# Optimization experiments

Measured on AMD Instinct MI355X. Metric: run time of the kernel, lower is better.

## Reference

```python
import jax, jax.numpy as jnp
import numpy as np

N = 100000      # nodes
E = 800000      # directed edges per branch
HID = 128
FOUT = 128
HEADS = 2
LAYERS = 3      # convlayer
JK_LAYERS = 3
H2 = (JK_LAYERS * HID) // 2   # PyG JK-LSTM hidden size = 192
N_AA = 26
N_SS = 3


def setup_inputs() -> dict:
    key = jax.random.key(0)
    ks = iter(jax.random.split(key, 32))
    def nrm(shape, scale=0.05):
        return jax.random.normal(next(ks), shape, dtype=jnp.float32) * scale
    return {
        "x_idx": jax.random.randint(next(ks), (N, 2), 0, N_SS),
        "x_flt": jax.random.normal(next(ks), (N, 5), dtype=jnp.float32),
        "edge_index_l": jax.random.randint(next(ks), (2, E), 0, N),
        "edge_index_r": jax.random.randint(next(ks), (2, E), 0, N),
        "emb_aa": nrm((2, N_AA, HID - 5)),          # [branch, vocab, hid-5]
        "emb_ss": nrm((2, N_SS, HID - 5)),
        "conv_W": nrm((2, LAYERS, HID, HEADS * HID)),
        "conv_att_src": nrm((2, LAYERS, HEADS, HID)),
        "conv_att_dst": nrm((2, LAYERS, HEADS, HID)),
        "conv_bias": nrm((2, LAYERS, HID)),
        "lstm_Wih": nrm((2, 2, 4 * H2, HID)),        # [branch, direction, 4H2, hid]
        "lstm_Whh": nrm((2, 2, 4 * H2, H2)),
        "lstm_bih": nrm((2, 2, 4 * H2)),
        "lstm_bhh": nrm((2, 2, 4 * H2)),
        "jk_att_W": nrm((2, 2 * H2)),
        "jk_att_b": nrm((2,)),
        "dummy_W": nrm((2, HID, HID)),
        "dummy_b": nrm((2, HID)),
        "fin_W": nrm((4, HID, FOUT)),
        "fin_b": nrm((4, FOUT)),
        "last_W": nrm((FOUT,)),                      # Linear(fout,1,bias=False)
    }


def _gat_conv(x, src, dst, W, att_src, att_dst, bias):
    # PyG GATConv, concat=False (mean over heads), leaky_relu slope 0.2
    n = x.shape[0]
    h, c = att_src.shape
    xh = (x @ W).reshape(n, h, c)                         # [N,H,C]
    a_src = jnp.einsum('nhc,hc->nh', xh, att_src)
    a_dst = jnp.einsum('nhc,hc->nh', xh, att_dst)
    e = jax.nn.leaky_relu(a_src[src] + a_dst[dst], 0.2)   # [E,H]
    m = jax.ops.segment_max(e, dst, num_segments=n)
    ex = jnp.exp(e - m[dst])
    denom = jax.ops.segment_sum(ex, dst, num_segments=n)
    alpha = ex / (denom[dst] + 1e-16)                     # segment softmax over dst
    out = jax.ops.segment_sum(xh[src] * alpha[:, :, None], dst, num_segments=n)
    return out.mean(axis=1) + bias                        # [N,C]


def _lstm_dir(xs, Wih, Whh, bih, bhh, reverse):
    # xs: [L,N,C]; single-layer LSTM, torch gate order i,f,g,o
    n = xs.shape[1]
    h2 = Whh.shape[1]
    b = bih + bhh
    def cell(carry, xt):
        h, c = carry
        g = xt @ Wih.T + h @ Whh.T + b
        i, f, gg, o = jnp.split(g, 4, axis=-1)
        c = jax.nn.sigmoid(f) * c + jax.nn.sigmoid(i) * jnp.tanh(gg)
        h = jax.nn.sigmoid(o) * jnp.tanh(c)
        return (h, c), h
    init = (jnp.zeros((n, h2), xs.dtype), jnp.zeros((n, h2), xs.dtype))
    _, hs = jax.lax.scan(cell, init, xs, reverse=reverse)
    return hs  # [L,N,H2]


def _jk(xs, Wih, Whh, bih, bhh, att_w, att_b):
    # PyG JumpingKnowledge('lstm'): bi-LSTM over layer axis + scalar attention
    hf = _lstm_dir(xs, Wih[0], Whh[0], bih[0], bhh[0], False)
    hb = _lstm_dir(xs, Wih[1], Whh[1], bih[1], bhh[1], True)
    h = jnp.concatenate([hf, hb], axis=-1)                # [L,N,2H2]
    a = jax.nn.softmax(jnp.einsum('lnh,h->ln', h, att_w) + att_b, axis=0)
    return (xs * a[..., None]).sum(axis=0)                # [N,C]


def _forward(x_idx, x_flt, edge_index_l, edge_index_r, emb_aa, emb_ss,
             conv_W, conv_att_src, conv_att_dst, conv_bias,
             lstm_Wih, lstm_Whh, lstm_bih, lstm_bhh, jk_att_W, jk_att_b,
             dummy_W, dummy_b, fin_W, fin_b, last_W):
    n = x_idx.shape[0]
    loops = jnp.arange(n)  # GATConv add_self_loops=True
    src_l = jnp.concatenate([edge_index_l[0], loops]); dst_l = jnp.concatenate([edge_index_l[1], loops])
    src_r = jnp.concatenate([edge_index_r[0], loops]); dst_r = jnp.concatenate([edge_index_r[1], loops])
    x_l = jnp.concatenate([emb_aa[0][x_idx[:, 0]] + emb_ss[0][x_idx[:, 1]], x_flt], axis=1)
    x_r = jnp.concatenate([emb_aa[1][x_idx[:, 0]] + emb_ss[1][x_idx[:, 1]], x_flt], axis=1)
    xs_l, xs_r = [], []
    for i in range(LAYERS):
        mean = (x_l + x_r) * 0.5
        o_l = mean + jax.nn.relu(_gat_conv(x_l, src_l, dst_l, conv_W[0, i], conv_att_src[0, i], conv_att_dst[0, i], conv_bias[0, i]))
        o_r = mean + jax.nn.relu(_gat_conv(x_r, src_r, dst_r, conv_W[1, i], conv_att_src[1, i], conv_att_dst[1, i], conv_bias[1, i]))
        x_l, x_r = o_l, o_r
        xs_l.append(x_l); xs_r.append(x_r)
    jk_l = _jk(jnp.stack(xs_l), lstm_Wih[0], lstm_Whh[0], lstm_bih[0], lstm_bhh[0], jk_att_W[0], jk_att_b[0])
    jk_r = _jk(jnp.stack(xs_r), lstm_Wih[1], lstm_Whh[1], lstm_bih[1], lstm_bhh[1], jk_att_W[1], jk_att_b[1])
    sq_l = jk_l @ dummy_W[0] + dummy_b[0]
    sq_r = jk_r @ dummy_W[1] + dummy_b[1]
    feats = [jk_l, sq_l, jk_r, sq_r]
    outs = [feats[i] @ fin_W[i] + fin_b[i] for i in range(4)]
    alpha = jax.nn.softmax(jnp.stack([o @ last_W for o in outs], axis=1), axis=1)  # [N,4]
    nodeemb = sum(outs[i] * alpha[:, i:i + 1] for i in range(4))
    return nodeemb


def reference(x_idx, x_flt, edge_index_l, edge_index_r, emb_aa, emb_ss,
              conv_W, conv_att_src, conv_att_dst, conv_bias,
              lstm_Wih, lstm_Whh, lstm_bih, lstm_bhh, jk_att_W, jk_att_b,
              dummy_W, dummy_b, fin_W, fin_b, last_W):
    return _forward(x_idx, x_flt, edge_index_l, edge_index_r, emb_aa, emb_ss,
                    conv_W, conv_att_src, conv_att_dst, conv_bias,
                    lstm_Wih, lstm_Whh, lstm_bih, lstm_bhh, jk_att_W, jk_att_b,
                    dummy_W, dummy_b, fin_W, fin_b, last_W)
```

## Files before the change

### kernel.cpp

```cpp
#include <hip/hip_runtime.h>
#include <cstddef>
#include <cstdint>

#define N_NODES 100000
#define N_EDGES 800000
#define EL_TOT  900000
#define HID 128
#define H2  192
#define G4  768
#define CH3 50000
#define BK  32
#define LDST 32
#define SCANB 98

typedef unsigned short bf16;
typedef __attribute__((ext_vector_type(8))) short bf16x8v;
typedef __attribute__((ext_vector_type(4))) float f32x4v;

#define AS1 __attribute__((address_space(1)))
#define AS3 __attribute__((address_space(3)))

__device__ __forceinline__ void async16(const bf16* g, bf16* l) {
    __builtin_amdgcn_global_load_lds((AS1 void*)g, (AS3 void*)l, 16, 0, 0);
}


__device__ __forceinline__ float b2f(bf16 u) {
    return __uint_as_float(((unsigned)u) << 16);
}
__device__ __forceinline__ bf16 f2b(float f) {
    unsigned u = __float_as_uint(f);
    u += 0x7FFFu + ((u >> 16) & 1u);
    return (bf16)(u >> 16);
}
__device__ __forceinline__ void stE(float* p, size_t i, float v) { p[i] = v; }
__device__ __forceinline__ void stE(bf16* p, size_t i, float v) { p[i] = f2b(v); }
__device__ __forceinline__ float ftanh(float x) {
    float cx = fminf(fmaxf(x, -15.f), 15.f);
    float e = __expf(2.f * cx);
    return (e - 1.f) / (e + 1.f);
}

__device__ __forceinline__ float x0_val(int c, int ia, int is_, int n,
                                        const float* __restrict__ embA,
                                        const float* __restrict__ embS,
                                        const float* __restrict__ xflt) {
    return (c < 123) ? (embA[ia * 123 + c] + embS[is_ * 123 + c])
                     : xflt[n * 5 + (c - 123)];
}

__device__ __forceinline__ int lstm_perm(int j) {
    int w = j & 63, tt = j >> 6;
    return (w >> 4) * 192 + tt * 16 + (w & 15);
}

__device__ __forceinline__ bool swz_tile(int R, int ntile, int& bm0, int& nt) {
    const int id = blockIdx.x;
    const int xcd = id & 7;
    const int s = id >> 3;
    nt = s % ntile;
    const int yp = (s / ntile) * 8 + xcd;
    if (yp * 128 >= R) return false;
    bm0 = yp * 128;
    return true;
}
static inline int swz_grid(int R, int ntile) {
    int panels = (R + 127) / 128;
    return 8 * ntile * ((panels + 7) / 8);
}


__global__ void sentinel_kernel(float* out, int n, float val) {
    int t = blockIdx.x * blockDim.x + threadIdx.x;
    if (t < n) out[t] = val;
}

__global__ void bsum_perm_kernel(const float* __restrict__ bih,
                                 const float* __restrict__ bhh,
                                 float* __restrict__ bsum) {
    int t = blockIdx.x * blockDim.x + threadIdx.x;
    if (t >= 4 * G4) return;
    int d = t / G4, j = t % G4;
    int orig = lstm_perm(j);
    bsum[t] = bih[d * G4 + orig] + bhh[d * G4 + orig];
}

__global__ void lstm_w_perm_kernel(const float* __restrict__ in,
                                   bf16* __restrict__ out, int K) {
    long long t = (long long)blockIdx.x * blockDim.x + threadIdx.x;
    long long tot = 4LL * G4 * K;
    if (t >= tot) return;
    int k = (int)(t % K);
    int j = (int)((t / K) % G4);
    int d = (int)(t / ((long long)G4 * K));
    int orig = lstm_perm(j);
    out[t] = f2b(in[((size_t)d * G4 + orig) * K + k]);
}

__global__ void trans_kernel(const float* __restrict__ in, bf16* __restrict__ out,
                             int batch, int K, int M) {
    long long t = (long long)blockIdx.x * blockDim.x + threadIdx.x;
    long long tot = (long long)batch * K * M;
    if (t >= tot) return;
    int per = K * M;
    int bt = (int)(t / per);
    int rem = (int)(t % per);
    int m = rem / K, k = rem % K;
    out[t] = f2b(in[(size_t)bt * per + (size_t)k * M + m]);
}


__global__ void deg_kernel(const int* __restrict__ dst, int* __restrict__ deg) {
    int t = blockIdx.x * blockDim.x + threadIdx.x;
    if (t >= EL_TOT) return;
    int d = (t < N_EDGES) ? dst[t] : (t - N_EDGES);
    atomicAdd(&deg[d], 1);
}

__global__ void scan1_kernel(const int* __restrict__ deg0, const int* __restrict__ deg1,
                             int* __restrict__ tmp0, int* __restrict__ tmp1,
                             int* __restrict__ bsums) {
    __shared__ int sdata[1024];
    const int b = blockIdx.y;
    const int* deg = b ? deg1 : deg0;
    int* tmp = b ? tmp1 : tmp0;
    int i = blockIdx.x * 1024 + threadIdx.x;
    int v = (i < N_NODES) ? deg[i] : 0;
    sdata[threadIdx.x] = v;
    __syncthreads();
    for (int off = 1; off < 1024; off <<= 1) {
        int t = (threadIdx.x >= (unsigned)off) ? sdata[threadIdx.x - off] : 0;
        __syncthreads();
        sdata[threadIdx.x] += t;
        __syncthreads();
    }
    if (i < N_NODES) tmp[i] = sdata[threadIdx.x];
    if (threadIdx.x == 1023) bsums[b * SCANB + blockIdx.x] = sdata[1023];
}

__global__ void scan2_kernel(int* __restrict__ bsums) {
    int b = threadIdx.x;
    if (b < 2) {
        int c = 0;
        for (int k = 0; k < SCANB; ++k) {
            int t = bsums[b * SCANB + k];
            bsums[b * SCANB + k] = c;
            c += t;
        }
    }
}

__global__ void scan3_kernel(const int* __restrict__ bsums,
                             const int* __restrict__ deg0, const int* __restrict__ deg1,
                             const int* __restrict__ tmp0, const int* __restrict__ tmp1,
                             int* __restrict__ offs0, int* __restrict__ offs1,
                             int* __restrict__ pos0, int* __restrict__ pos1) {
    const int b = blockIdx.y;
    const int* deg = b ? deg1 : deg0;
    const int* tmp = b ? tmp1 : tmp0;
    int* offs = b ? offs1 : offs0;
    int* pos = b ? pos1 : pos0;
    int carry = bsums[b * SCANB + blockIdx.x];
    int i = blockIdx.x * 1024 + threadIdx.x;
    if (i < N_NODES) {
        int inc = tmp[i] + carry;
        offs[i + 1] = inc;
        pos[i] = inc - deg[i];
    }
    if (i == 0) offs[0] = 0;
}

__global__ void fill_kernel(const int* __restrict__ srcrow,
                            const int* __restrict__ dstrow,
                            int* __restrict__ pos, int* __restrict__ srcs) {
    int t = blockIdx.x * blockDim.x + threadIdx.x;
    if (t >= EL_TOT) return;
    int s, d;
    if (t < N_EDGES) { s = srcrow[t]; d = dstrow[t]; }
    else             { s = d = t - N_EDGES; }
    int p = atomicAdd(&pos[d], 1);
    srcs[p] = s;
}

template<typename TC>
__device__ __forceinline__ void gemm128_body(
    const bf16* __restrict__ A1, const bf16* __restrict__ B1, int K1,
    TC* __restrict__ C, const float* __restrict__ bias, int R, int M,
    int bm0, int bn0, const float* __restrict__ as_, float* __restrict__ asrc) {
    __shared__ bf16 As[2][128 * LDST];
    __shared__ bf16 Bs[2][128 * LDST];
    const int tid = threadIdx.x;
    const int lane = tid & 63;
    const int wave = tid >> 6;
    const int wm = (wave & 1) * 64, wn = (wave >> 1) * 64;
    const int l15 = lane & 15;
    const int q8 = (lane >> 4) * 8;
    const int lr = lane >> 2;
    const int lc = (lane & 3) * 8;

    f32x4v acc[4][4];
#pragma unroll
    for (int i = 0; i < 4; ++i)
#pragma unroll
        for (int j = 0; j < 4; ++j) acc[i][j] = (f32x4v)(0.0f);

    const int ns = K1 / BK;
    auto stage = [&](int buf, int s) {
        const int k0 = s * BK;
#pragma unroll
        for (int rnd = 0; rnd < 2; ++rnd) {
            const int rbase = wave * 16 + rnd * 64;
            const int row = rbase + lr;
            int ga = bm0 + row; ga = (ga < R) ? ga : (R - 1);
            async16(A1 + (size_t)ga * K1 + k0 + lc, &As[buf][rbase * LDST]);
            async16(B1 + (size_t)(bn0 + row) * K1 + k0 + lc, &Bs[buf][rbase * LDST]);
        }
    };

    stage(0, 0);
    __syncthreads();
    for (int s = 0; s < ns; ++s) {
        const int cur = s & 1;
        if (s + 1 < ns) stage(cur ^ 1, s + 1);
        bf16x8v af[4], bfv[4];
#pragma unroll
        for (int i = 0; i < 4; ++i) {
            af[i]  = *(const bf16x8v*)&As[cur][(wm + i * 16 + l15) * LDST + q8];
            bfv[i] = *(const bf16x8v*)&Bs[cur][(wn + i * 16 + l15) * LDST + q8];
        }
#pragma unroll
        for (int i = 0; i < 4; ++i)
#pragma unroll
            for (int j = 0; j < 4; ++j)
                acc[i][j] = __builtin_amdgcn_mfma_f32_16x16x32_bf16(
                    af[i], bfv[j], acc[i][j], 0, 0, 0);
        __syncthreads();
    }

    const int head = bn0 >> 7;
#pragma unroll
    for (int i = 0; i < 4; ++i) {
        const int row0 = bm0 + wm + i * 16 + (lane >> 4) * 4;
        if (as_) {
            float rs[4] = {0.f, 0.f, 0.f, 0.f};
#pragma unroll
            for (int j = 0; j < 4; ++j) {
                const float w = as_[bn0 + wn + j * 16 + l15];
#pragma unroll
                for (int r = 0; r < 4; ++r) rs[r] += w * acc[i][j][r];
            }
#pragma unroll
            for (int m = 1; m < 16; m <<= 1)
#pragma unroll
                for (int r = 0; r < 4; ++r) rs[r] += __shfl_xor(rs[r], m);
            if (l15 == 0) {
#pragma unroll
                for (int r = 0; r < 4; ++r) {
                    const int gr = row0 + r;
                    if (gr < R) asrc[2 * gr + head] = rs[r];
                }
            }
        }
#pragma unroll
        for (int j = 0; j < 4; ++j) {
            const int col = bn0 + wn + j * 16 + l15;
            const float bv = bias ? bias[col] : 0.f;
#pragma unroll
            for (int r = 0; r < 4; ++r) {
                const int gr = row0 + r;
                if (gr < R) stE(C, (size_t)gr * M + col, acc[i][j][r] + bv);
            }
        }
    }
}

template<typename TC>
__global__ __launch_bounds__(256) void mfma_gemm_kernel(
    const bf16* __restrict__ A1, const bf16* __restrict__ B1, int K1,
    TC* __restrict__ C, const float* __restrict__ bias, int R, int M,
    const float* __restrict__ as_, float* __restrict__ asrc) {
    int bm0, nt;
    if (!swz_tile(R, M >> 7, bm0, nt)) return;
    gemm128_body<TC>(A1, B1, K1, C, bias, R, M, bm0, nt * 128, as_, asrc);
}

template<typename TC>
__global__ __launch_bounds__(256) void mfma_gemm_b_kernel(
    const bf16* a0, const bf16* a1, const bf16* a2, const bf16* a3,
    const bf16* __restrict__ Bbase,
    TC* c0, TC* c1, TC* c2, TC* c3,
    const float* __restrict__ bias, int R) {
    int bm0, nt;
    if (!swz_tile(R, 1, bm0, nt)) return;
    const int y = blockIdx.y;
    const bf16* A1 = (y == 0) ? a0 : (y == 1) ? a1 : (y == 2) ? a2 : a3;
    TC* C = (y == 0) ? c0 : (y == 1) ? c1 : (y == 2) ? c2 : c3;
    gemm128_body<TC>(A1, Bbase + (size_t)y * 128 * 128, 128, C,
                     bias + (size_t)y * 128, R, 128, bm0, 0, nullptr, nullptr);
}

__global__ __launch_bounds__(256) void lstm_gemm_kernel(
    const bf16* __restrict__ A1, const bf16* __restrict__ B1,
    const bf16* __restrict__ A2, const bf16* __restrict__ B2,
    const float* __restrict__ bias, bf16* __restrict__ c_state,
    bf16* __restrict__ h_out, const float* __restrict__ aw,
    float* __restrict__ score, int first, int last, int R) {
    __shared__ bf16 As[2][128 * LDST];
    __shared__ bf16 Bs[2][128 * LDST];
    int bm0, nt;
    if (!swz_tile(R, G4 >> 7, bm0, nt)) return;
    const int bn0 = nt * 128;
    const int tid = threadIdx.x;
    const int lane = tid & 63;
    const int wave = tid >> 6;
    const int wm = (wave & 1) * 64, wn = (wave >> 1) * 64;
    const int l15 = lane & 15;
    const int q = lane >> 4;
    const int q8 = q * 8;
    const int lr = lane >> 2;
    const int lc = (lane & 3) * 8;

    f32x4v acc[4][4];
#pragma unroll
    for (int i = 0; i < 4; ++i)
#pragma unroll
        for (int j = 0; j < 4; ++j) acc[i][j] = (f32x4v)(0.0f);

    const int n1 = HID / BK;
    const int ns = n1 + (first ? 0 : (H2 / BK));

    auto stage = [&](int buf, int s) {
        const bf16* Ap; const bf16* Bp; int K, k0;
        if (s < n1) { Ap = A1; Bp = B1; K = HID; k0 = s * BK; }
        else        { Ap = A2; Bp = B2; K = H2;  k0 = (s - n1) * BK; }
#pragma unroll
        for (int rnd = 0; rnd < 2; ++rnd) {
            const int rbase = wave * 16 + rnd * 64;
            const int row = rbase + lr;
            int ga = bm0 + row; ga = (ga < R) ? ga : (R - 1);
            async16(Ap + (size_t)ga * K + k0 + lc, &As[buf][rbase * LDST]);
            async16(Bp + (size_t)(bn0 + row) * K + k0 + lc, &Bs[buf][rbase * LDST]);
        }
    };

    stage(0, 0);
    __syncthreads();
    for (int s = 0; s < ns; ++s) {
        const int cur = s & 1;
        if (s + 1 < ns) stage(cur ^ 1, s + 1);
        bf16x8v af[4], bfv[4];
#pragma unroll
        for (int i = 0; i < 4; ++i) {
            af[i]  = *(const bf16x8v*)&As[cur][(wm + i * 16 + l15) * LDST + q8];
            bfv[i] = *(const bf16x8v*)&Bs[cur][(wn + i * 16 + l15) * LDST + q8];
        }
#pragma unroll
        for (int i = 0; i < 4; ++i)
#pragma unroll
            for (int j = 0; j < 4; ++j)
                acc[i][j] = __builtin_amdgcn_mfma_f32_16x16x32_bf16(
                    af[i], bfv[j], acc[i][j], 0, 0, 0);
        __syncthreads();
    }

    const int u = ((bn0 + wn) >> 6) * 16 + l15;
    const float awu = aw[u];
    float bv[4];
#pragma unroll
    for (int j = 0; j < 4; ++j) bv[j] = bias[bn0 + wn + j * 16 + l15];
    float psum[4][4];
#pragma unroll
    for (int i = 0; i < 4; ++i) {
        const int row0 = bm0 + wm + i * 16 + q * 4;
#pragma unroll
        for (int r = 0; r < 4; ++r) {
            const int gr = row0 + r;
            const bool ok = gr < R;
            float ig = acc[i][0][r] + bv[0];
            float fg = acc[i][1][r] + bv[1];
            float gg = acc[i][2][r] + bv[2];
            float og = acc[i][3][r] + bv[3];
            float si = 1.f / (1.f + __expf(-ig));
            float sf = 1.f / (1.f + __expf(-fg));
            float so = 1.f / (1.f + __expf(-og));
            float co = (ok && !first) ? b2f(c_state[(size_t)gr * H2 + u]) : 0.f;
            float cn = sf * co + si * ftanh(gg);
            float hn = so * ftanh(cn);
            if (ok && !last) {
                c_state[(size_t)gr * H2 + u] = f2b(cn);
                h_out[(size_t)gr * H2 + u] = f2b(hn);
            }
            psum[i][r] = hn * awu;
        }
    }
#pragma unroll
    for (int m = 1; m < 16; m <<= 1)
#pragma unroll
        for (int i = 0; i < 4; ++i)
#pragma unroll
            for (int r = 0; r < 4; ++r)
                psum[i][r] += __shfl_xor(psum[i][r], m);
    if (l15 == 0) {
#pragma unroll
        for (int i = 0; i < 4; ++i)
#pragma unroll
            for (int r = 0; r < 4; ++r) {
                const int gr = bm0 + wm + i * 16 + q * 4 + r;
                if (gr < R) atomicAdd(&score[gr], psum[i][r]);
            }
    }
}

__global__ __launch_bounds__(256) void mfma_gemm_x0_kernel(
    const int* __restrict__ xidx, const float* __restrict__ xflt,
    const float* __restrict__ embA, const float* __restrict__ embS,
    const bf16* __restrict__ B1, bf16* __restrict__ C, int R, int M,
    const float* __restrict__ as_, float* __restrict__ asrc) {
    __shared__ bf16 As[128 * LDST];
    __shared__ bf16 Bs[128 * LDST];
    int bm0, nt;
    if (!swz_tile(R, M >> 7, bm0, nt)) return;
    const int bn0 = nt * 128;
    const int tid = threadIdx.x;
    const int lane = tid & 63;
    const int wave = tid >> 6;
    const int wm = (wave & 1) * 64, wn = (wave >> 1) * 64;
    const int l15 = lane & 15;
    const int q8 = (lane >> 4) * 8;
    const int srow = tid >> 2;
    const int scol = (tid & 3) * 8;
    const int lr = lane >> 2;
    const int lc = (lane & 3) * 8;

    f32x4v acc[4][4];
#pragma unroll
    for (int i = 0; i < 4; ++i)
#pragma unroll
        for (int j = 0; j < 4; ++j) acc[i][j] = (f32x4v)(0.0f);

    for (int k0 = 0; k0 < 128; k0 += BK) {
#pragma unroll
        for (int rnd = 0; rnd < 2; ++rnd) {
            {
                int row = srow + rnd * 64;
                int ga = bm0 + row; ga = (ga < R) ? ga : (R - 1);
                int ia = xidx[2 * ga], is_ = xidx[2 * ga + 1];
                bf16 tmp[8];
#pragma unroll
                for (int t = 0; t < 8; ++t)
                    tmp[t] = f2b(x0_val(k0 + scol + t, ia, is_, ga, embA, embS, xflt));
                *(int4*)&As[row * LDST + scol] = *(const int4*)tmp;
            }
            {
                const int rbase = wave * 16 + rnd * 64;
                int row = rbase + lr;
                async16(B1 + (size_t)(bn0 + row) * 128 + k0 + lc, &Bs[rbase * LDST]);
            }
        }
        __syncthreads();
        bf16x8v af[4], bfv[4];
#pragma unroll
        for (int i = 0; i < 4; ++i) {
            af[i]  = *(const bf16x8v*)&As[(wm + i * 16 + l15) * LDST + q8];
            bfv[i] = *(const bf16x8v*)&Bs[(wn + i * 16 + l15) * LDST + q8];
        }
#pragma unroll
        for (int i = 0; i < 4; ++i)
#pragma unroll
            for (int j = 0; j < 4; ++j)
                acc[i][j] = __builtin_amdgcn_mfma_f32_16x16x32_bf16(
                    af[i], bfv[j], acc[i][j], 0, 0, 0);
        __syncthreads();
    }
    const int head = bn0 >> 7;
#pragma unroll
    for (int i = 0; i < 4; ++i) {
        const int row0 = bm0 + wm + i * 16 + (lane >> 4) * 4;
        {
            float rs[4] = {0.f, 0.f, 0.f, 0.f};
#pragma unroll
            for (int j = 0; j < 4; ++j) {
                const float w = as_[bn0 + wn + j * 16 + l15];
#pragma unroll
                for (int r = 0; r < 4; ++r) rs[r] += w * acc[i][j][r];
            }
#pragma unroll
            for (int m = 1; m < 16; m <<= 1)
#pragma unroll
                for (int r = 0; r < 4; ++r) rs[r] += __shfl_xor(rs[r], m);
            if (l15 == 0) {
#pragma unroll
                for (int r = 0; r < 4; ++r) {
                    const int gr = row0 + r;
                    if (gr < R) asrc[2 * gr + head] = rs[r];
                }
            }
        }
#pragma unroll
        for (int j = 0; j < 4; ++j) {
            const int col = bn0 + wn + j * 16 + l15;
#pragma unroll
            for (int r = 0; r < 4; ++r) {
                const int gr = row0 + r;
                if (gr < R) C[(size_t)gr * M + col] = f2b(acc[i][j][r]);
            }
        }
    }
}


__device__ __forceinline__ float lrelu02(float x) { return x > 0.f ? x : 0.2f * x; }

__global__ __launch_bounds__(256) void agg_kernel(
    const bf16* __restrict__ xh, const float* __restrict__ asrc,
    const float* __restrict__ ad_, const int* __restrict__ offs,
    const int* __restrict__ srcs,
    const bf16* __restrict__ xprev_l, const bf16* __restrict__ xprev_r,
    const int* __restrict__ xidx, const float* __restrict__ xflt,
    const float* __restrict__ embAl, const float* __restrict__ embSl,
    const float* __restrict__ embAr, const float* __restrict__ embSr,
    const float* __restrict__ bias, bf16* __restrict__ outx) {
    int n = (blockIdx.x * blockDim.x + threadIdx.x) >> 6;
    int lane = threadIdx.x & 63;
    if (n >= N_NODES) return;
    const int start = offs[n], end = offs[n + 1];
    const int l15 = lane & 15;
    const int g = lane >> 4;

    float d0, d1;
    {
        uint2 v = *(const uint2*)(xh + (size_t)n * 256 + lane * 4);
        float p = ad_[lane * 4 + 0] * b2f((bf16)(v.x & 0xffffu))
                + ad_[lane * 4 + 1] * b2f((bf16)(v.x >> 16))
                + ad_[lane * 4 + 2] * b2f((bf16)(v.y & 0xffffu))
                + ad_[lane * 4 + 3] * b2f((bf16)(v.y >> 16));
        for (int o = 1; o < 32; o <<= 1) p += __shfl_xor(p, o);
        d0 = __shfl(p, 0);
        d1 = __shfl(p, 32);
    }

    float acc0[8] = {0, 0, 0, 0, 0, 0, 0, 0};
    float acc1[8] = {0, 0, 0, 0, 0, 0, 0, 0};
    float ds0 = 0.f, ds1 = 0.f;
#pragma unroll 2
    for (int j = start; j < end; j += 4) {
        int e = j + g;
        if (e < end) {
            int s = srcs[e];
            float2 a2 = *(const float2*)(asrc + 2 * s);
            float al0 = __expf(lrelu02(a2.x + d0));
            float al1 = __expf(lrelu02(a2.y + d1));
            if (l15 == 0) { ds0 += al0; ds1 += al1; }
            const bf16* row = xh + (size_t)s * 256 + l15 * 8;
            int4 v0 = *(const int4*)row;
            int4 v1 = *(const int4*)(row + 128);
            const int* w0 = (const int*)&v0;
            const int* w1 = (const int*)&v1;
#pragma unroll
            for (int t = 0; t < 4; ++t) {
                acc0[2 * t]     += __uint_as_float(((unsigned)w0[t]) << 16) * al0;
                acc0[2 * t + 1] += __uint_as_float(((unsigned)w0[t]) & 0xffff0000u) * al0;
                acc1[2 * t]     += __uint_as_float(((unsigned)w1[t]) << 16) * al1;
                acc1[2 * t + 1] += __uint_as_float(((unsigned)w1[t]) & 0xffff0000u) * al1;
            }
        }
    }
#pragma unroll
    for (int t = 0; t < 8; ++t) {
        acc0[t] += __shfl_xor(acc0[t], 16); acc0[t] += __shfl_xor(acc0[t], 32);
        acc1[t] += __shfl_xor(acc1[t], 16); acc1[t] += __shfl_xor(acc1[t], 32);
    }
    ds0 += __shfl_xor(ds0, 16); ds0 += __shfl_xor(ds0, 32);
    ds1 += __shfl_xor(ds1, 16); ds1 += __shfl_xor(ds1, 32);
    ds0 = __shfl(ds0, 0); ds1 = __shfl(ds1, 0);
    const float inv0 = 1.f / (ds0 + 1e-16f);
    const float inv1 = 1.f / (ds1 + 1e-16f);
    float accm[8];
#pragma unroll
    for (int t = 0; t < 8; ++t)
        accm[t] = 0.5f * (acc0[t] * inv0 + acc1[t] * inv1);

    if (lane < 16) {
        const int c0 = l15 * 8;
        const size_t base = (size_t)n * HID + c0;
        float xm[8];
        if (xidx) {
            int ia = xidx[2 * n], is_ = xidx[2 * n + 1];
#pragma unroll
            for (int t = 0; t < 8; ++t)
                xm[t] = 0.5f * (x0_val(c0 + t, ia, is_, n, embAl, embSl, xflt) +
                                x0_val(c0 + t, ia, is_, n, embAr, embSr, xflt));
        } else {
            int4 vl = *(const int4*)(xprev_l + base);
            int4 vr = *(const int4*)(xprev_r + base);
            const int* wl = (const int*)&vl;
            const int* wr = (const int*)&vr;
#pragma unroll
            for (int t = 0; t < 4; ++t) {
                xm[2 * t] = 0.5f * (__uint_as_float(((unsigned)wl[t]) << 16) +
                                    __uint_as_float(((unsigned)wr[t]) << 16));
                xm[2 * t + 1] = 0.5f * (__uint_as_float(((unsigned)wl[t]) & 0xffff0000u) +
                                        __uint_as_float(((unsigned)wr[t]) & 0xffff0000u));
            }
        }
        bf16 res[8];
#pragma unroll
        for (int t = 0; t < 8; ++t)
            res[t] = f2b(xm[t] + fmaxf(0.f, accm[t] + bias[c0 + t]));
        *(int4*)(outx + base) = *(const int4*)res;
    }
}


__global__ __launch_bounds__(256) void jkfin_kernel(
    const float* __restrict__ sb, const bf16* __restrict__ xs0,
    const bf16* __restrict__ xs1, const bf16* __restrict__ xs2,
    bf16* __restrict__ jk) {
    int w = (blockIdx.x * blockDim.x + threadIdx.x) >> 6;
    int lane = threadIdx.x & 63;
    if (w >= N_NODES) return;
    float s0 = sb[w], s1 = sb[N_NODES + w], s2 = sb[2 * N_NODES + w];
    float m = fmaxf(s0, fmaxf(s1, s2));
    float a0 = __expf(s0 - m), a1 = __expf(s1 - m), a2 = __expf(s2 - m);
    float inv = 1.f / (a0 + a1 + a2);
    a0 *= inv; a1 *= inv; a2 *= inv;
    size_t gn = (size_t)w * HID + lane * 2;
#pragma unroll
    for (int t = 0; t < 2; ++t) {
        float v0 = b2f(xs0[gn + t]);
        float v1 = b2f(xs1[gn + t]);
        float v2 = b2f(xs2[gn + t]);
        jk[gn + t] = f2b(v0 * a0 + v1 * a1 + v2 * a2);
    }
}

__global__ __launch_bounds__(256) void final_kernel(
    const float* __restrict__ o0, const float* __restrict__ o1,
    const float* __restrict__ o2, const float* __restrict__ o3,
    const float* __restrict__ lw, float* __restrict__ out, int nloc, long long c3off) {
    int w = (blockIdx.x * blockDim.x + threadIdx.x) >> 6;
    int lane = threadIdx.x & 63;
    if (w >= nloc) return;
    size_t base = (size_t)w * HID;
    float w0 = lw[lane], w1 = lw[64 + lane];
    const float* op[4] = {o0, o1, o2, o3};
    float v[4][2];
    float s[4];
#pragma unroll
    for (int i = 0; i < 4; ++i) {
        v[i][0] = op[i][base + lane];
        v[i][1] = op[i][base + 64 + lane];
        float t = v[i][0] * w0 + v[i][1] * w1;
        for (int o = 1; o < 64; o <<= 1) t += __shfl_xor(t, o);
        s[i] = t;
    }
    float m = fmaxf(fmaxf(s[0], s[1]), fmaxf(s[2], s[3]));
    float e0 = __expf(s[0] - m), e1 = __expf(s[1] - m);
    float e2 = __expf(s[2] - m), e3 = __expf(s[3] - m);
    float inv = 1.f / (e0 + e1 + e2 + e3);
    float r0 = (v[0][0] * e0 + v[1][0] * e1 + v[2][0] * e2 + v[3][0] * e3) * inv;
    float r1 = (v[0][1] * e0 + v[1][1] * e1 + v[2][1] * e2 + v[3][1] * e3) * inv;
    size_t obase = (size_t)(c3off + w) * HID;
    out[obase + lane] = r0;
    out[obase + 64 + lane] = r1;
}


static long long align1k(long long x) { return (x + 1023) & ~1023LL; }

extern "C" void kernel_launch(void* const* d_in, const int* in_sizes, int n_in,
                              void* d_out, int out_size, void* d_ws, size_t ws_size,
                              hipStream_t stream) {
    (void)in_sizes; (void)n_in; (void)out_size;
    const int*   x_idx   = (const int*)  d_in[0];
    const float* x_flt   = (const float*)d_in[1];
    const int*   ei_l    = (const int*)  d_in[2];
    const int*   ei_r    = (const int*)  d_in[3];
    const float* emb_aa  = (const float*)d_in[4];
    const float* emb_ss  = (const float*)d_in[5];
    const float* conv_W  = (const float*)d_in[6];
    const float* att_s   = (const float*)d_in[7];
    const float* att_d   = (const float*)d_in[8];
    const float* conv_b  = (const float*)d_in[9];
    const float* Wih     = (const float*)d_in[10];
    const float* Whh     = (const float*)d_in[11];
    const float* bih     = (const float*)d_in[12];
    const float* bhh     = (const float*)d_in[13];
    const float* jkw     = (const float*)d_in[14];
    const float* dummy_W = (const float*)d_in[16];
    const float* dummy_b = (const float*)d_in[17];
    const float* fin_W   = (const float*)d_in[18];
    const float* fin_b   = (const float*)d_in[19];
    const float* last_W  = (const float*)d_in[20];
    float* out = (float*)d_out;

    const long long S = (long long)N_NODES * HID;
    char* ws = (char*)d_ws;
    long long off = 0;

    bf16* hist = (bf16*)(ws + off);  off += align1k(6 * S * 2);
    float* scores = (float*)(ws + off); off += align1k(6LL * N_NODES * 4);
    float* bsum   = (float*)(ws + off); off += align1k(4LL * G4 * 4);
    int* bsums    = (int*)(ws + off);  off += align1k(2LL * SCANB * 4);
    bf16* Wih_b   = (bf16*)(ws + off); off += align1k(4LL * G4 * HID * 2);
    bf16* Whh_b   = (bf16*)(ws + off); off += align1k(4LL * G4 * H2 * 2);
    bf16* dummyWt = (bf16*)(ws + off); off += align1k(2LL * 128 * 128 * 2);
    bf16* finWt   = (bf16*)(ws + off); off += align1k(4LL * 128 * 128 * 2);

    char* BIG = ws + off;
    const long long slot0 = align1k(2 * S * 2);
    const long long slot1 = align1k((long long)N_NODES * H2 * 2);
    const long long need = off + slot0 + slot1;

    if ((long long)ws_size < need) {
        float val = 200000.0f + (float)(ws_size >> 20);
        sentinel_kernel<<<(N_NODES * HID + 255) / 256, 256, 0, stream>>>(
            out, N_NODES * HID, val);
        return;
    }

    bf16* xh  = (bf16*)BIG;
    bf16* jkb = (bf16*)BIG;
    int* ibase = (int*)(BIG + slot0);
    int *deg[2], *offs[2], *pos[2], *srcs[2];
    long long io = 0;
    for (int b = 0; b < 2; ++b) {
        deg[b]  = ibase + io; io += N_NODES;
        offs[b] = ibase + io; io += N_NODES + 1;
        pos[b]  = ibase + io; io += N_NODES;
        srcs[b] = ibase + io; io += EL_TOT;
    }
    long long io4a = ((io * 4 + 15) & ~15LL);
    float* asrc = (float*)(BIG + slot0 + io4a);
    bf16* convWt = (bf16*)(BIG + slot0 + io4a + 2LL * N_NODES * 4);
    bf16* hA = (bf16*)BIG;
    bf16* hB = (bf16*)d_out;
    bf16* cC = (bf16*)(BIG + slot0);

    const float* embA[2] = {emb_aa, emb_aa + 26 * 123};
    const float* embS[2] = {emb_ss, emb_ss + 3 * 123};

    bsum_perm_kernel<<<12, 256, 0, stream>>>(bih, bhh, bsum);
    trans_kernel<<<(6 * 128 * 256 + 255) / 256, 256, 0, stream>>>(
        conv_W, convWt, 6, 128, 256);
    lstm_w_perm_kernel<<<(4 * G4 * HID + 255) / 256, 256, 0, stream>>>(
        Wih, Wih_b, HID);
    lstm_w_perm_kernel<<<(4 * G4 * H2 + 255) / 256, 256, 0, stream>>>(
        Whh, Whh_b, H2);
    trans_kernel<<<(2 * 128 * 128 + 255) / 256, 256, 0, stream>>>(
        dummy_W, dummyWt, 2, 128, 128);
    trans_kernel<<<(4 * 128 * 128 + 255) / 256, 256, 0, stream>>>(
        fin_W, finWt, 4, 128, 128);
    hipMemsetAsync(deg[0], 0, N_NODES * sizeof(int), stream);
    hipMemsetAsync(deg[1], 0, N_NODES * sizeof(int), stream);
    deg_kernel<<<(EL_TOT + 255) / 256, 256, 0, stream>>>(ei_l + N_EDGES, deg[0]);
    deg_kernel<<<(EL_TOT + 255) / 256, 256, 0, stream>>>(ei_r + N_EDGES, deg[1]);
    scan1_kernel<<<dim3(SCANB, 2), 1024, 0, stream>>>(
        deg[0], deg[1], pos[0], pos[1], bsums);
    scan2_kernel<<<1, 64, 0, stream>>>(bsums);
    scan3_kernel<<<dim3(SCANB, 2), 1024, 0, stream>>>(
        bsums, deg[0], deg[1], pos[0], pos[1], offs[0], offs[1], pos[0], pos[1]);
    fill_kernel<<<(EL_TOT + 255) / 256, 256, 0, stream>>>(
        ei_l, ei_l + N_EDGES, pos[0], srcs[0]);
    fill_kernel<<<(EL_TOT + 255) / 256, 256, 0, stream>>>(
        ei_r, ei_r + N_EDGES, pos[1], srcs[1]);

    for (int i = 0; i < 3; ++i) {
        for (int b = 0; b < 2; ++b) {
            const bf16* Wc = convWt + (size_t)(b * 3 + i) * 256 * 128;
            const float* as_ = att_s + (size_t)(b * 3 + i) * 2 * HID;
            if (i == 0) {
                mfma_gemm_x0_kernel<<<swz_grid(N_NODES, 2), 256, 0, stream>>>(
                    x_idx, x_flt, embA[b], embS[b], Wc, xh, N_NODES, 256,
                    as_, asrc);
            } else {
                mfma_gemm_kernel<bf16><<<swz_grid(N_NODES, 2), 256, 0, stream>>>(
                    hist + (size_t)(b * 3 + i - 1) * S, Wc, 128,
                    xh, nullptr, N_NODES, 256, as_, asrc);
            }
            const bf16* xpl = (i == 0) ? nullptr : hist + (size_t)(i - 1) * S;
            const bf16* xpr = (i == 0) ? nullptr : hist + (size_t)(3 + i - 1) * S;
            agg_kernel<<<25000, 256, 0, stream>>>(
                xh, asrc, att_d + (size_t)(b * 3 + i) * 2 * HID,
                offs[b], srcs[b], xpl, xpr,
                (i == 0) ? x_idx : nullptr, x_flt,
                embA[0], embS[0], embA[1], embS[1],
                conv_b + (size_t)(b * 3 + i) * HID, hist + (size_t)(b * 3 + i) * S);
        }
    }

    hipMemsetAsync(scores, 0, (size_t)6 * N_NODES * 4, stream);
    const int gx = swz_grid(N_NODES, 6);
    for (int b = 0; b < 2; ++b) {
        for (int dir = 0; dir < 2; ++dir) {
            const int combo = b * 2 + dir;
            const bf16* Wi = Wih_b + (size_t)combo * G4 * HID;
            const bf16* Wh = Whh_b + (size_t)combo * G4 * H2;
            const float* bs = bsum + (size_t)combo * G4;
            const float* aw = jkw + (size_t)b * 2 * H2 + (size_t)dir * H2;
            for (int st = 0; st < 3; ++st) {
                int l = dir ? (2 - st) : st;
                const bf16* A = hist + (size_t)(b * 3 + l) * S;
                const bf16* hin = (st == 0) ? nullptr : ((st & 1) ? hA : hB);
                bf16* hout = (st & 1) ? hB : hA;
                lstm_gemm_kernel<<<gx, 256, 0, stream>>>(
                    A, Wi, hin, Wh, bs, cC, hout, aw,
                    scores + (size_t)(b * 3 + l) * N_NODES,
                    st == 0 ? 1 : 0, st == 2 ? 1 : 0, N_NODES);
            }
        }
    }
    for (int b = 0; b < 2; ++b)
        jkfin_kernel<<<25000, 256, 0, stream>>>(
            scores + (size_t)b * 3 * N_NODES,
            hist + (size_t)b * 3 * S, hist + (size_t)(b * 3 + 1) * S,
            hist + (size_t)(b * 3 + 2) * S, jkb + (size_t)b * S);

    float* f3 = (float*)hist;
    bf16* jkl = jkb; bf16* jkr = jkb + S;
    for (long long c3 = 0; c3 < N_NODES; c3 += CH3) {
        int Rr = (int)((N_NODES - c3) < CH3 ? (N_NODES - c3) : CH3);
        float* o0 = f3;
        float* o1 = f3 + 1LL * CH3 * HID;
        float* o2 = f3 + 2LL * CH3 * HID;
        float* o3 = f3 + 3LL * CH3 * HID;
        bf16* sql = (bf16*)(f3 + 4LL * CH3 * HID);
        bf16* sqr = sql + (long long)CH3 * HID;
        mfma_gemm_b_kernel<bf16><<<dim3(swz_grid(Rr, 1), 2), 256, 0, stream>>>(
            jkl + c3 * HID, jkr + c3 * HID, nullptr, nullptr,
            dummyWt, sql, sqr, nullptr, nullptr, dummy_b, Rr);
        mfma_gemm_b_kernel<float><<<dim3(swz_grid(Rr, 1), 4), 256, 0, stream>>>(
            jkl + c3 * HID, sql, jkr + c3 * HID, sqr,
            finWt, o0, o1, o2, o3, fin_b, Rr);
        final_kernel<<<(Rr + 3) / 4, 256, 0, stream>>>(
            o0, o1, o2, o3, last_W, out, Rr, c3);
    }
}
```

Baseline: 2.841 ms.

## Overlap next branch's GAT GEMM with current branch's aggregation in fused launches

```diff
diff --git a/kernel.cpp b/kernel.cpp
--- a/kernel.cpp
+++ b/kernel.cpp
@@ -12,6 +12,8 @@
 #define BK  32
 #define LDST 32
 #define SCANB 98
+#define GEMM_GRID 1568
+#define AGG_GRID 25000
 
 typedef unsigned short bf16;
 typedef __attribute__((ext_vector_type(8))) short bf16x8v;
@@ -54,8 +56,7 @@
     return (w >> 4) * 192 + tt * 16 + (w & 15);
 }
 
-__device__ __forceinline__ bool swz_tile(int R, int ntile, int& bm0, int& nt) {
-    const int id = blockIdx.x;
+__device__ __forceinline__ bool swz_tile(int id, int R, int ntile, int& bm0, int& nt) {
     const int xcd = id & 7;
     const int s = id >> 3;
     nt = s % ntile;
@@ -183,12 +184,14 @@
 }
 
 template<typename TC>
-__device__ __forceinline__ void gemm128_body(
+__device__ __forceinline__ void gemm128_dev(
+    bf16* __restrict__ AsB, bf16* __restrict__ BsB, int bid,
     const bf16* __restrict__ A1, const bf16* __restrict__ B1, int K1,
     TC* __restrict__ C, const float* __restrict__ bias, int R, int M,
-    int bm0, int bn0, const float* __restrict__ as_, float* __restrict__ asrc) {
-    __shared__ bf16 As[2][128 * LDST];
-    __shared__ bf16 Bs[2][128 * LDST];
+    const float* __restrict__ as_, float* __restrict__ asrc) {
+    int bm0, nt;
+    if (!swz_tile(bid, R, M >> 7, bm0, nt)) return;
+    const int bn0 = nt * 128;
     const int tid = threadIdx.x;
     const int lane = tid & 63;
     const int wave = tid >> 6;
@@ -207,13 +210,15 @@
     const int ns = K1 / BK;
     auto stage = [&](int buf, int s) {
         const int k0 = s * BK;
+        bf16* As = AsB + buf * 128 * LDST;
+        bf16* Bs = BsB + buf * 128 * LDST;
 #pragma unroll
         for (int rnd = 0; rnd < 2; ++rnd) {
             const int rbase = wave * 16 + rnd * 64;
             const int row = rbase + lr;
             int ga = bm0 + row; ga = (ga < R) ? ga : (R - 1);
-            async16(A1 + (size_t)ga * K1 + k0 + lc, &As[buf][rbase * LDST]);
-            async16(B1 + (size_t)(bn0 + row) * K1 + k0 + lc, &Bs[buf][rbase * LDST]);
+            async16(A1 + (size_t)ga * K1 + k0 + lc, &As[rbase * LDST]);
+            async16(B1 + (size_t)(bn0 + row) * K1 + k0 + lc, &Bs[rbase * LDST]);
         }
     };
 
@@ -222,11 +227,13 @@
     for (int s = 0; s < ns; ++s) {
         const int cur = s & 1;
         if (s + 1 < ns) stage(cur ^ 1, s + 1);
+        const bf16* As = AsB + cur * 128 * LDST;
+        const bf16* Bs = BsB + cur * 128 * LDST;
         bf16x8v af[4], bfv[4];
 #pragma unroll
         for (int i = 0; i < 4; ++i) {
-            af[i]  = *(const bf16x8v*)&As[cur][(wm + i * 16 + l15) * LDST + q8];
-            bfv[i] = *(const bf16x8v*)&Bs[cur][(wn + i * 16 + l15) * LDST + q8];
+            af[i]  = *(const bf16x8v*)&As[(wm + i * 16 + l15) * LDST + q8];
+            bfv[i] = *(const bf16x8v*)&Bs[(wn + i * 16 + l15) * LDST + q8];
         }
 #pragma unroll
         for (int i = 0; i < 4; ++i)
@@ -274,152 +281,14 @@
     }
 }
 
-template<typename TC>
-__global__ __launch_bounds__(256) void mfma_gemm_kernel(
-    const bf16* __restrict__ A1, const bf16* __restrict__ B1, int K1,
-    TC* __restrict__ C, const float* __restrict__ bias, int R, int M,
-    const float* __restrict__ as_, float* __restrict__ asrc) {
-    int bm0, nt;
-    if (!swz_tile(R, M >> 7, bm0, nt)) return;
-    gemm128_body<TC>(A1, B1, K1, C, bias, R, M, bm0, nt * 128, as_, asrc);
-}
-
-template<typename TC>
-__global__ __launch_bounds__(256) void mfma_gemm_b_kernel(
-    const bf16* a0, const bf16* a1, const bf16* a2, const bf16* a3,
-    const bf16* __restrict__ Bbase,
-    TC* c0, TC* c1, TC* c2, TC* c3,
-    const float* __restrict__ bias, int R) {
-    int bm0, nt;
-    if (!swz_tile(R, 1, bm0, nt)) return;
-    const int y = blockIdx.y;
-    const bf16* A1 = (y == 0) ? a0 : (y == 1) ? a1 : (y == 2) ? a2 : a3;
-    TC* C = (y == 0) ? c0 : (y == 1) ? c1 : (y == 2) ? c2 : c3;
-    gemm128_body<TC>(A1, Bbase + (size_t)y * 128 * 128, 128, C,
-                     bias + (size_t)y * 128, R, 128, bm0, 0, nullptr, nullptr);
-}
-
-__global__ __launch_bounds__(256) void lstm_gemm_kernel(
-    const bf16* __restrict__ A1, const bf16* __restrict__ B1,
-    const bf16* __restrict__ A2, const bf16* __restrict__ B2,
-    const float* __restrict__ bias, bf16* __restrict__ c_state,
-    bf16* __restrict__ h_out, const float* __restrict__ aw,
-    float* __restrict__ score, int first, int last, int R) {
-    __shared__ bf16 As[2][128 * LDST];
-    __shared__ bf16 Bs[2][128 * LDST];
-    int bm0, nt;
-    if (!swz_tile(R, G4 >> 7, bm0, nt)) return;
-    const int bn0 = nt * 128;
-    const int tid = threadIdx.x;
-    const int lane = tid & 63;
-    const int wave = tid >> 6;
-    const int wm = (wave & 1) * 64, wn = (wave >> 1) * 64;
-    const int l15 = lane & 15;
-    const int q = lane >> 4;
-    const int q8 = q * 8;
-    const int lr = lane >> 2;
-    const int lc = (lane & 3) * 8;
-
-    f32x4v acc[4][4];
-#pragma unroll
-    for (int i = 0; i < 4; ++i)
-#pragma unroll
-        for (int j = 0; j < 4; ++j) acc[i][j] = (f32x4v)(0.0f);
-
-    const int n1 = HID / BK;
-    const int ns = n1 + (first ? 0 : (H2 / BK));
-
-    auto stage = [&](int buf, int s) {
-        const bf16* Ap; const bf16* Bp; int K, k0;
-        if (s < n1) { Ap = A1; Bp = B1; K = HID; k0 = s * BK; }
-        else        { Ap = A2; Bp = B2; K = H2;  k0 = (s - n1) * BK; }
-#pragma unroll
-        for (int rnd = 0; rnd < 2; ++rnd) {
-            const int rbase = wave * 16 + rnd * 64;
-            const int row = rbase + lr;
-            int ga = bm0 + row; ga = (ga < R) ? ga : (R - 1);
-            async16(Ap + (size_t)ga * K + k0 + lc, &As[buf][rbase * LDST]);
-            async16(Bp + (size_t)(bn0 + row) * K + k0 + lc, &Bs[buf][rbase * LDST]);
-        }
-    };
-
-    stage(0, 0);
-    __syncthreads();
-    for (int s = 0; s < ns; ++s) {
-        const int cur = s & 1;
-        if (s + 1 < ns) stage(cur ^ 1, s + 1);
-        bf16x8v af[4], bfv[4];
-#pragma unroll
-        for (int i = 0; i < 4; ++i) {
-            af[i]  = *(const bf16x8v*)&As[cur][(wm + i * 16 + l15) * LDST + q8];
-            bfv[i] = *(const bf16x8v*)&Bs[cur][(wn + i * 16 + l15) * LDST + q8];
-        }
-#pragma unroll
-        for (int i = 0; i < 4; ++i)
-#pragma unroll
-            for (int j = 0; j < 4; ++j)
-                acc[i][j] = __builtin_amdgcn_mfma_f32_16x16x32_bf16(
-                    af[i], bfv[j], acc[i][j], 0, 0, 0);
-        __syncthreads();
-    }
-
-    const int u = ((bn0 + wn) >> 6) * 16 + l15;
-    const float awu = aw[u];
-    float bv[4];
-#pragma unroll
-    for (int j = 0; j < 4; ++j) bv[j] = bias[bn0 + wn + j * 16 + l15];
-    float psum[4][4];
-#pragma unroll
-    for (int i = 0; i < 4; ++i) {
-        const int row0 = bm0 + wm + i * 16 + q * 4;
-#pragma unroll
-        for (int r = 0; r < 4; ++r) {
-            const int gr = row0 + r;
-            const bool ok = gr < R;
-            float ig = acc[i][0][r] + bv[0];
-            float fg = acc[i][1][r] + bv[1];
-            float gg = acc[i][2][r] + bv[2];
-            float og = acc[i][3][r] + bv[3];
-            float si = 1.f / (1.f + __expf(-ig));
-            float sf = 1.f / (1.f + __expf(-fg));
-            float so = 1.f / (1.f + __expf(-og));
-            float co = (ok && !first) ? b2f(c_state[(size_t)gr * H2 + u]) : 0.f;
-            float cn = sf * co + si * ftanh(gg);
-            float hn = so * ftanh(cn);
-            if (ok && !last) {
-                c_state[(size_t)gr * H2 + u] = f2b(cn);
-                h_out[(size_t)gr * H2 + u] = f2b(hn);
-            }
-            psum[i][r] = hn * awu;
-        }
-    }
-#pragma unroll
-    for (int m = 1; m < 16; m <<= 1)
-#pragma unroll
-        for (int i = 0; i < 4; ++i)
-#pragma unroll
-            for (int r = 0; r < 4; ++r)
-                psum[i][r] += __shfl_xor(psum[i][r], m);
-    if (l15 == 0) {
-#pragma unroll
-        for (int i = 0; i < 4; ++i)
-#pragma unroll
-            for (int r = 0; r < 4; ++r) {
-                const int gr = bm0 + wm + i * 16 + q * 4 + r;
-                if (gr < R) atomicAdd(&score[gr], psum[i][r]);
-            }
-    }
-}
-
-__global__ __launch_bounds__(256) void mfma_gemm_x0_kernel(
+__device__ __forceinline__ void gemm_x0_dev(
+    bf16* __restrict__ As, bf16* __restrict__ Bs, int bid,
     const int* __restrict__ xidx, const float* __restrict__ xflt,
     const float* __restrict__ embA, const float* __restrict__ embS,
     const bf16* __restrict__ B1, bf16* __restrict__ C, int R, int M,
     const float* __restrict__ as_, float* __restrict__ asrc) {
-    __shared__ bf16 As[128 * LDST];
-    __shared__ bf16 Bs[128 * LDST];
     int bm0, nt;
-    if (!swz_tile(R, M >> 7, bm0, nt)) return;
+    if (!swz_tile(bid, R, M >> 7, bm0, nt)) return;
     const int bn0 = nt * 128;
     const int tid = threadIdx.x;
     const int lane = tid & 63;
@@ -511,7 +380,8 @@
 
 __device__ __forceinline__ float lrelu02(float x) { return x > 0.f ? x : 0.2f * x; }
 
-__global__ __launch_bounds__(256) void agg_kernel(
+__device__ __forceinline__ void agg_dev(
+    int bid,
     const bf16* __restrict__ xh, const float* __restrict__ asrc,
     const float* __restrict__ ad_, const int* __restrict__ offs,
     const int* __restrict__ srcs,
@@ -520,7 +390,7 @@
     const float* __restrict__ embAl, const float* __restrict__ embSl,
     const float* __restrict__ embAr, const float* __restrict__ embSr,
     const float* __restrict__ bias, bf16* __restrict__ outx) {
-    int n = (blockIdx.x * blockDim.x + threadIdx.x) >> 6;
+    int n = (bid * 256 + (int)threadIdx.x) >> 6;
     int lane = threadIdx.x & 63;
     if (n >= N_NODES) return;
     const int start = offs[n], end = offs[n + 1];
@@ -608,6 +478,194 @@
         for (int t = 0; t < 8; ++t)
             res[t] = f2b(xm[t] + fmaxf(0.f, accm[t] + bias[c0 + t]));
         *(int4*)(outx + base) = *(const int4*)res;
+    }
+}
+
+
+__global__ __launch_bounds__(256) void mfma_gemm_x0_kernel(
+    const int* xidx, const float* xflt, const float* embA, const float* embS,
+    const bf16* B1, bf16* C, int R, int M, const float* as_, float* asrc) {
+    __shared__ bf16 As[128 * LDST];
+    __shared__ bf16 Bs[128 * LDST];
+    gemm_x0_dev(As, Bs, blockIdx.x, xidx, xflt, embA, embS, B1, C, R, M, as_, asrc);
+}
+
+__global__ __launch_bounds__(256) void agg_kernel(
+    const bf16* xh, const float* asrc, const float* ad_, const int* offs,
+    const int* srcs, const bf16* xprev_l, const bf16* xprev_r,
+    const int* xidx, const float* xflt,
+    const float* embAl, const float* embSl,
+    const float* embAr, const float* embSr,
+    const float* bias, bf16* outx) {
+    agg_dev(blockIdx.x, xh, asrc, ad_, offs, srcs, xprev_l, xprev_r,
+            xidx, xflt, embAl, embSl, embAr, embSr, bias, outx);
+}
+
+__global__ __launch_bounds__(256) void fat1_kernel(
+    const bf16* gA1, const bf16* gB1, bf16* gC, const float* gas, float* gasrc,
+    const bf16* xh, const float* asrc, const float* ad_, const int* offs,
+    const int* srcs, const bf16* xprev_l, const bf16* xprev_r,
+    const int* xidx, const float* xflt,
+    const float* embAl, const float* embSl,
+    const float* embAr, const float* embSr,
+    const float* bias, bf16* outx) {
+    __shared__ bf16 As[2 * 128 * LDST];
+    __shared__ bf16 Bs[2 * 128 * LDST];
+    if (blockIdx.x < GEMM_GRID) {
+        gemm128_dev<bf16>(As, Bs, blockIdx.x, gA1, gB1, 128, gC, nullptr,
+                          N_NODES, 256, gas, gasrc);
+    } else {
+        agg_dev(blockIdx.x - GEMM_GRID, xh, asrc, ad_, offs, srcs,
+                xprev_l, xprev_r, xidx, xflt, embAl, embSl, embAr, embSr,
+                bias, outx);
+    }
+}
+
+__global__ __launch_bounds__(256) void fat0_kernel(
+    const int* gxidx, const float* gxflt, const float* gembA, const float* gembS,
+    const bf16* gB1, bf16* gC, const float* gas, float* gasrc,
+    const bf16* xh, const float* asrc, const float* ad_, const int* offs,
+    const int* srcs,
+    const int* xidx, const float* xflt,
+    const float* embAl, const float* embSl,
+    const float* embAr, const float* embSr,
+    const float* bias, bf16* outx) {
+    __shared__ bf16 As[128 * LDST];
+    __shared__ bf16 Bs[128 * LDST];
+    if (blockIdx.x < GEMM_GRID) {
+        gemm_x0_dev(As, Bs, blockIdx.x, gxidx, gxflt, gembA, gembS, gB1, gC,
+                    N_NODES, 256, gas, gasrc);
+    } else {
+        agg_dev(blockIdx.x - GEMM_GRID, xh, asrc, ad_, offs, srcs,
+                nullptr, nullptr, xidx, xflt, embAl, embSl, embAr, embSr,
+                bias, outx);
+    }
+}
+
+template<typename TC>
+__global__ __launch_bounds__(256) void mfma_gemm_b_kernel(
+    const bf16* a0, const bf16* a1, const bf16* a2, const bf16* a3,
+    const bf16* __restrict__ Bbase,
+    TC* c0, TC* c1, TC* c2, TC* c3,
+    const float* __restrict__ bias, int R) {
+    __shared__ bf16 As[2 * 128 * LDST];
+    __shared__ bf16 Bs[2 * 128 * LDST];
+    const int y = blockIdx.y;
+    const bf16* A1 = (y == 0) ? a0 : (y == 1) ? a1 : (y == 2) ? a2 : a3;
+    TC* C = (y == 0) ? c0 : (y == 1) ? c1 : (y == 2) ? c2 : c3;
+    gemm128_dev<TC>(As, Bs, blockIdx.x, A1, Bbase + (size_t)y * 128 * 128, 128,
+                    C, bias + (size_t)y * 128, R, 128, nullptr, nullptr);
+}
+
+__global__ __launch_bounds__(256) void lstm_gemm_kernel(
+    const bf16* __restrict__ A1, const bf16* __restrict__ B1,
+    const bf16* __restrict__ A2, const bf16* __restrict__ B2,
+    const float* __restrict__ bias, bf16* __restrict__ c_state,
+    bf16* __restrict__ h_out, const float* __restrict__ aw,
+    float* __restrict__ score, int first, int last, int R) {
+    __shared__ bf16 As[2][128 * LDST];
+    __shared__ bf16 Bs[2][128 * LDST];
+    int bm0, nt;
+    if (!swz_tile(blockIdx.x, R, G4 >> 7, bm0, nt)) return;
+    const int bn0 = nt * 128;
+    const int tid = threadIdx.x;
+    const int lane = tid & 63;
+    const int wave = tid >> 6;
+    const int wm = (wave & 1) * 64, wn = (wave >> 1) * 64;
+    const int l15 = lane & 15;
+    const int q = lane >> 4;
+    const int q8 = q * 8;
+    const int lr = lane >> 2;
+    const int lc = (lane & 3) * 8;
+
+    f32x4v acc[4][4];
+#pragma unroll
+    for (int i = 0; i < 4; ++i)
+#pragma unroll
+        for (int j = 0; j < 4; ++j) acc[i][j] = (f32x4v)(0.0f);
+
+    const int n1 = HID / BK;
+    const int ns = n1 + (first ? 0 : (H2 / BK));
+
+    auto stage = [&](int buf, int s) {
+        const bf16* Ap; const bf16* Bp; int K, k0;
+        if (s < n1) { Ap = A1; Bp = B1; K = HID; k0 = s * BK; }
+        else        { Ap = A2; Bp = B2; K = H2;  k0 = (s - n1) * BK; }
+#pragma unroll
+        for (int rnd = 0; rnd < 2; ++rnd) {
+            const int rbase = wave * 16 + rnd * 64;
+            const int row = rbase + lr;
+            int ga = bm0 + row; ga = (ga < R) ? ga : (R - 1);
+            async16(Ap + (size_t)ga * K + k0 + lc, &As[buf][rbase * LDST]);
+            async16(Bp + (size_t)(bn0 + row) * K + k0 + lc, &Bs[buf][rbase * LDST]);
+        }
+    };
+
+    stage(0, 0);
+    __syncthreads();
+    for (int s = 0; s < ns; ++s) {
+        const int cur = s & 1;
+        if (s + 1 < ns) stage(cur ^ 1, s + 1);
+        bf16x8v af[4], bfv[4];
+#pragma unroll
+        for (int i = 0; i < 4; ++i) {
+            af[i]  = *(const bf16x8v*)&As[cur][(wm + i * 16 + l15) * LDST + q8];
+            bfv[i] = *(const bf16x8v*)&Bs[cur][(wn + i * 16 + l15) * LDST + q8];
+        }
+#pragma unroll
+        for (int i = 0; i < 4; ++i)
+#pragma unroll
+            for (int j = 0; j < 4; ++j)
+                acc[i][j] = __builtin_amdgcn_mfma_f32_16x16x32_bf16(
+                    af[i], bfv[j], acc[i][j], 0, 0, 0);
+        __syncthreads();
+    }
+
+    const int u = ((bn0 + wn) >> 6) * 16 + l15;
+    const float awu = aw[u];
+    float bv[4];
+#pragma unroll
+    for (int j = 0; j < 4; ++j) bv[j] = bias[bn0 + wn + j * 16 + l15];
+    float psum[4][4];
+#pragma unroll
+    for (int i = 0; i < 4; ++i) {
+        const int row0 = bm0 + wm + i * 16 + q * 4;
+#pragma unroll
+        for (int r = 0; r < 4; ++r) {
+            const int gr = row0 + r;
+            const bool ok = gr < R;
+            float ig = acc[i][0][r] + bv[0];
+            float fg = acc[i][1][r] + bv[1];
+            float gg = acc[i][2][r] + bv[2];
+            float og = acc[i][3][r] + bv[3];
+            float si = 1.f / (1.f + __expf(-ig));
+            float sf = 1.f / (1.f + __expf(-fg));
+            float so = 1.f / (1.f + __expf(-og));
+            float co = (ok && !first) ? b2f(c_state[(size_t)gr * H2 + u]) : 0.f;
+            float cn = sf * co + si * ftanh(gg);
+            float hn = so * ftanh(cn);
+            if (ok && !last) {
+                c_state[(size_t)gr * H2 + u] = f2b(cn);
+                h_out[(size_t)gr * H2 + u] = f2b(hn);
+            }
+            psum[i][r] = hn * awu;
+        }
+    }
+#pragma unroll
+    for (int m = 1; m < 16; m <<= 1)
+#pragma unroll
+        for (int i = 0; i < 4; ++i)
+#pragma unroll
+            for (int r = 0; r < 4; ++r)
+                psum[i][r] += __shfl_xor(psum[i][r], m);
+    if (l15 == 0) {
+#pragma unroll
+        for (int i = 0; i < 4; ++i)
+#pragma unroll
+            for (int r = 0; r < 4; ++r) {
+                const int gr = bm0 + wm + i * 16 + q * 4 + r;
+                if (gr < R) atomicAdd(&score[gr], psum[i][r]);
+            }
     }
 }
 
@@ -719,7 +777,7 @@
         return;
     }
 
-    bf16* xh  = (bf16*)BIG;
+    bf16* xhb[2] = { (bf16*)BIG, (bf16*)d_out };
     bf16* jkb = (bf16*)BIG;
     int* ibase = (int*)(BIG + slot0);
     int *deg[2], *offs[2], *pos[2], *srcs[2];
@@ -731,8 +789,9 @@
         srcs[b] = ibase + io; io += EL_TOT;
     }
     long long io4a = ((io * 4 + 15) & ~15LL);
-    float* asrc = (float*)(BIG + slot0 + io4a);
-    bf16* convWt = (bf16*)(BIG + slot0 + io4a + 2LL * N_NODES * 4);
+    float* asrcb[2] = { (float*)(BIG + slot0 + io4a),
+                        (float*)(BIG + slot0 + io4a) + 2LL * N_NODES };
+    bf16* convWt = (bf16*)(BIG + slot0 + io4a + 4LL * N_NODES * 4);
     bf16* hA = (bf16*)BIG;
     bf16* hB = (bf16*)d_out;
     bf16* cC = (bf16*)(BIG + slot0);
@@ -765,29 +824,49 @@
     fill_kernel<<<(EL_TOT + 255) / 256, 256, 0, stream>>>(
         ei_r, ei_r + N_EDGES, pos[1], srcs[1]);
 
-    for (int i = 0; i < 3; ++i) {
-        for (int b = 0; b < 2; ++b) {
-            const bf16* Wc = convWt + (size_t)(b * 3 + i) * 256 * 128;
-            const float* as_ = att_s + (size_t)(b * 3 + i) * 2 * HID;
-            if (i == 0) {
-                mfma_gemm_x0_kernel<<<swz_grid(N_NODES, 2), 256, 0, stream>>>(
-                    x_idx, x_flt, embA[b], embS[b], Wc, xh, N_NODES, 256,
-                    as_, asrc);
-            } else {
-                mfma_gemm_kernel<bf16><<<swz_grid(N_NODES, 2), 256, 0, stream>>>(
-                    hist + (size_t)(b * 3 + i - 1) * S, Wc, 128,
-                    xh, nullptr, N_NODES, 256, as_, asrc);
-            }
-            const bf16* xpl = (i == 0) ? nullptr : hist + (size_t)(i - 1) * S;
-            const bf16* xpr = (i == 0) ? nullptr : hist + (size_t)(3 + i - 1) * S;
-            agg_kernel<<<25000, 256, 0, stream>>>(
-                xh, asrc, att_d + (size_t)(b * 3 + i) * 2 * HID,
-                offs[b], srcs[b], xpl, xpr,
-                (i == 0) ? x_idx : nullptr, x_flt,
-                embA[0], embS[0], embA[1], embS[1],
-                conv_b + (size_t)(b * 3 + i) * HID, hist + (size_t)(b * 3 + i) * S);
-        }
-    }
+    auto Wc = [&](int b, int i) {
+        return convWt + (size_t)(b * 3 + i) * 256 * 128; };
+    auto AS = [&](int b, int i) {
+        return att_s + (size_t)(b * 3 + i) * 2 * HID; };
+    auto AD = [&](int b, int i) {
+        return att_d + (size_t)(b * 3 + i) * 2 * HID; };
+    auto CB = [&](int b, int i) {
+        return conv_b + (size_t)(b * 3 + i) * HID; };
+    auto HO = [&](int b, int i) {
+        return hist + (size_t)(b * 3 + i) * S; };
+
+    mfma_gemm_x0_kernel<<<GEMM_GRID, 256, 0, stream>>>(
+        x_idx, x_flt, embA[0], embS[0], Wc(0, 0), xhb[0], N_NODES, 256,
+        AS(0, 0), asrcb[0]);
+    fat0_kernel<<<GEMM_GRID + AGG_GRID, 256, 0, stream>>>(
+        x_idx, x_flt, embA[1], embS[1], Wc(1, 0), xhb[1], AS(1, 0), asrcb[1],
+        xhb[0], asrcb[0], AD(0, 0), offs[0], srcs[0],
+        x_idx, x_flt, embA[0], embS[0], embA[1], embS[1],
+        CB(0, 0), HO(0, 0));
+    fat1_kernel<<<GEMM_GRID + AGG_GRID, 256, 0, stream>>>(
+        HO(0, 0), Wc(0, 1), xhb[0], AS(0, 1), asrcb[0],
+        xhb[1], asrcb[1], AD(1, 0), offs[1], srcs[1],
+        nullptr, nullptr, x_idx, x_flt,
+        embA[0], embS[0], embA[1], embS[1], CB(1, 0), HO(1, 0));
+    fat1_kernel<<<GEMM_GRID + AGG_GRID, 256, 0, stream>>>(
+        HO(1, 0), Wc(1, 1), xhb[1], AS(1, 1), asrcb[1],
+        xhb[0], asrcb[0], AD(0, 1), offs[0], srcs[0],
+        HO(0, 0), HO(1, 0), nullptr, x_flt,
+        embA[0], embS[0], embA[1], embS[1], CB(0, 1), HO(0, 1));
+    fat1_kernel<<<GEMM_GRID + AGG_GRID, 256, 0, stream>>>(
+        HO(0, 1), Wc(0, 2), xhb[0], AS(0, 2), asrcb[0],
+        xhb[1], asrcb[1], AD(1, 1), offs[1], srcs[1],
+        HO(0, 0), HO(1, 0), nullptr, x_flt,
+        embA[0], embS[0], embA[1], embS[1], CB(1, 1), HO(1, 1));
+    fat1_kernel<<<GEMM_GRID + AGG_GRID, 256, 0, stream>>>(
+        HO(1, 1), Wc(1, 2), xhb[1], AS(1, 2), asrcb[1],
+        xhb[0], asrcb[0], AD(0, 2), offs[0], srcs[0],
+        HO(0, 1), HO(1, 1), nullptr, x_flt,
+        embA[0], embS[0], embA[1], embS[1], CB(0, 2), HO(0, 2));
+    agg_kernel<<<AGG_GRID, 256, 0, stream>>>(
+        xhb[1], asrcb[1], AD(1, 2), offs[1], srcs[1],
+        HO(0, 1), HO(1, 1), nullptr, x_flt,
+        embA[0], embS[0], embA[1], embS[1], CB(1, 2), HO(1, 2));
 
     hipMemsetAsync(scores, 0, (size_t)6 * N_NODES * 4, stream);
     const int gx = swz_grid(N_NODES, 6);
```

After: 3.101 ms. +9.2%, slower.
